# Optimization experiments

Measured on AMD Instinct MI355X. Metric: run time of the kernel, lower is better.

Reference implementation:

```python
import jax, jax.numpy as jnp
import numpy as np

D_MODEL = 1024
D_STATE = 16
D_CONV = 4
EXPAND = 2
D_INNER = EXPAND * D_MODEL  # 2048
BATCH = 2
SEQ = 2048


def setup_inputs() -> dict:
    key = jax.random.key(0)
    ks = jax.random.split(key, 7)
    s = 0.02
    x = jax.random.normal(ks[0], (BATCH, SEQ, D_MODEL), jnp.float32)
    in_proj_w = jax.random.normal(ks[1], (2 * D_INNER, D_MODEL), jnp.float32) * s
    conv_w = jax.random.normal(ks[2], (D_INNER, 1, D_CONV), jnp.float32) * s  # depthwise: groups=d_inner
    conv_b = jnp.zeros((D_INNER,), jnp.float32)
    x_proj_w = jax.random.normal(ks[3], (2 * D_STATE, D_INNER), jnp.float32) * s
    dt_proj_w = jax.random.normal(ks[4], (D_INNER, D_INNER), jnp.float32) * s
    dt_proj_b = jnp.zeros((D_INNER,), jnp.float32)
    # A = arange(1..d_state) repeated for each inner channel; A_log = log(A)
    A_log = jnp.log(jnp.tile(jnp.arange(1, D_STATE + 1, dtype=jnp.float32), (D_INNER, 1)))
    D_param = jnp.ones((D_INNER,), jnp.float32)
    out_proj_w = jax.random.normal(ks[5], (D_MODEL, D_INNER), jnp.float32) * s
    return {"x": x, "in_proj_w": in_proj_w, "conv_w": conv_w, "conv_b": conv_b,
            "x_proj_w": x_proj_w, "dt_proj_w": dt_proj_w, "dt_proj_b": dt_proj_b,
            "A_log": A_log, "D_param": D_param, "out_proj_w": out_proj_w}


def reference(x, in_proj_w, conv_w, conv_b, x_proj_w, dt_proj_w, dt_proj_b, A_log, D_param, out_proj_w):
    B, L, _ = x.shape
    # input projection -> [B, L, 2*d_inner], split into ssm path and gate
    xz = x @ in_proj_w.T
    x_ssm, z = jnp.split(xz, 2, axis=-1)

    # causal depthwise conv1d (torch pads both sides by d_conv-1 then slices [:L])
    xc = jnp.transpose(x_ssm, (0, 2, 1))  # [B, d_inner, L]
    xc = jnp.pad(xc, ((0, 0), (0, 0), (D_CONV - 1, 0)))
    xc = jax.lax.conv_general_dilated(
        xc, conv_w, window_strides=(1,), padding='VALID',
        dimension_numbers=('NCH', 'OIH', 'NCH'), feature_group_count=D_INNER)
    xc = xc + conv_b[None, :, None]
    x_act = jax.nn.silu(jnp.transpose(xc, (0, 2, 1)))  # [B, L, d_inner]

    delta = jax.nn.softplus(x_act @ dt_proj_w.T + dt_proj_b)  # [B, L, d_inner]
    bc = x_act @ x_proj_w.T                                   # [B, L, 2*d_state]
    B_p, C_p = jnp.split(bc, 2, axis=-1)

    A = -jnp.exp(A_log)  # [d_inner, d_state]

    def step(h, inp):
        u_i, d_i, B_i, C_i = inp  # [B,d], [B,d], [B,n], [B,n]
        dA = jnp.exp(d_i[..., None] * A)                       # [B, d, n]
        h = dA * h + (d_i * u_i)[..., None] * B_i[:, None, :]  # [B, d, n]
        y = jnp.einsum('bdn,bn->bd', h, C_i)
        return h, y

    h0 = jnp.zeros((B, D_INNER, D_STATE), x.dtype)
    seq = (jnp.swapaxes(x_act, 0, 1), jnp.swapaxes(delta, 0, 1),
           jnp.swapaxes(B_p, 0, 1), jnp.swapaxes(C_p, 0, 1))
    _, ys = jax.lax.scan(step, h0, seq)  # ys: [L, B, d_inner]
    y_ssm = jnp.swapaxes(ys, 0, 1) + x_act * D_param

    y = y_ssm * jax.nn.silu(z)
    return y @ out_proj_w.T
```

## Files before the change

### kernel.cpp

```cpp
#include <hip/hip_runtime.h>
#include <hip/hip_bf16.h>
#include <math.h>

#define DM 1024
#define DS 16
#define DI 2048
#define NB 2
#define LL 2048
#define BL (NB*LL)
#define LC 32
#define NC (LL/LC)

typedef __attribute__((ext_vector_type(8))) short short8;
typedef __attribute__((ext_vector_type(8))) unsigned short ushort8;
typedef __attribute__((ext_vector_type(4))) float f32x4;

__device__ __forceinline__ float silu_f(float x){ return x / (1.f + __expf(-x)); }
__device__ __forceinline__ float softplus_f(float x){ return (x > 15.f) ? x : log1pf(__expf(x)); }
__device__ __forceinline__ unsigned short f2bf(float f){
  unsigned u = __float_as_uint(f);
  u += 0x7fff + ((u >> 16) & 1);
  return (unsigned short)(u >> 16);
}
__device__ __forceinline__ float bf2f(unsigned short v){
  return __uint_as_float(((unsigned)v) << 16);
}

__global__ __launch_bounds__(256) void f2b_k(const float* __restrict__ src,
                                             unsigned short* __restrict__ dst, int n)
{
  int i = (blockIdx.x * 256 + threadIdx.x) * 8;
  if (i >= n) return;
  float4 v0 = *(const float4*)&src[i];
  float4 v1 = *(const float4*)&src[i + 4];
  ushort8 o;
  o[0]=f2bf(v0.x); o[1]=f2bf(v0.y); o[2]=f2bf(v0.z); o[3]=f2bf(v0.w);
  o[4]=f2bf(v1.x); o[5]=f2bf(v1.y); o[6]=f2bf(v1.z); o[7]=f2bf(v1.w);
  *(ushort8*)&dst[i] = o;
}

__global__ __launch_bounds__(256) void f2b_multi(
    const float* __restrict__ s0, unsigned short* __restrict__ d0, int c0,
    const float* __restrict__ s1, unsigned short* __restrict__ d1, int c1,
    const float* __restrict__ s2, unsigned short* __restrict__ d2, int c2,
    const float* __restrict__ s3, unsigned short* __restrict__ d3, int c3)
{
  int b = blockIdx.x;
  const float* s; unsigned short* d;
  if (b < c0)              { s = s0; d = d0; }
  else if ((b -= c0) < c1) { s = s1; d = d1; }
  else if ((b -= c1) < c2) { s = s2; d = d2; }
  else                     { b -= c2; s = s3; d = d3; }
  int i = (b * 256 + threadIdx.x) * 8;
  float4 v0 = *(const float4*)&s[i];
  float4 v1 = *(const float4*)&s[i + 4];
  ushort8 o;
  o[0]=f2bf(v0.x); o[1]=f2bf(v0.y); o[2]=f2bf(v0.z); o[3]=f2bf(v0.w);
  o[4]=f2bf(v1.x); o[5]=f2bf(v1.y); o[6]=f2bf(v1.z); o[7]=f2bf(v1.w);
  *(ushort8*)&d[i] = o;
}

template<int EPI, int OUTBF>
__global__ __launch_bounds__(512, 1) void gemm5(
    const unsigned short* __restrict__ A, const unsigned short* __restrict__ Bw,
    const float* __restrict__ bias, void* __restrict__ Cp,
    int N, int K)
{
  constexpr int BM = 128, BN = 256;
  __shared__ unsigned short lds[2][(BM + BN) * 64];
  const int t0 = threadIdx.x;
  const int wid = t0 >> 6, lane = t0 & 63;
  const int nbx = N / BN;
  const int cpx = (int)gridDim.x >> 3;
  const int bid = (int)blockIdx.x;
  const int swz = (bid & 7) * cpx + (bid >> 3);
  const int bm = (swz / nbx) * BM, bn = (swz % nbx) * BN;
  const int wm = (wid >> 2) * 64, wn = (wid & 3) * 64;

  f32x4 acc[4][4] = {};

  auto stage = [&](int buf, int kt) {
    const int k0 = kt * 64;
    #pragma unroll
    for (int s = 0; s < 6; s++) {
      int g = wid * 6 + s;
      int row = g * 8 + (lane >> 3);
      int ch  = (lane & 7) ^ (lane >> 3);
      const unsigned short* src;
      if (g < 16) src = A  + (size_t)(bm + row) * K + k0 + ch * 8;
      else        src = Bw + (size_t)(bn + row - BM) * K + k0 + ch * 8;
      __builtin_amdgcn_global_load_lds(
          (const __attribute__((address_space(1))) void*)src,
          (__attribute__((address_space(3))) void*)(&lds[buf][(size_t)g * 512]), 16, 0, 0);
    }
  };

  stage(0, 0);
  stage(1, 1);
  asm volatile("s_waitcnt vmcnt(6)" ::: "memory");
  __builtin_amdgcn_s_barrier();

  const int nk = K >> 6;

#define G5_READS(Q)                                                          \
  short8 af[2][4], bfr[2][4];                                                \
  _Pragma("unroll")                                                          \
  for (int ks = 0; ks < 2; ks++) {                                           \
    int cc = ((ks << 2) + (lane >> 4)) ^ (lane & 7);                         \
    _Pragma("unroll")                                                        \
    for (int i = 0; i < 4; i++) {                                            \
      af[ks][i]  = *(const short8*)&lds[Q][(wm + i * 16 + (lane & 15)) * 64 + cc * 8]; \
      bfr[ks][i] = *(const short8*)&lds[Q][BM * 64 + (wn + i * 16 + (lane & 15)) * 64 + cc * 8]; \
    }                                                                        \
  }

#define G5_MFMA()                                                            \
  _Pragma("unroll")                                                          \
  for (int ks = 0; ks < 2; ks++)                                             \
    _Pragma("unroll")                                                        \
    for (int i = 0; i < 4; i++)                                              \
      _Pragma("unroll")                                                      \
      for (int j = 0; j < 4; j++)                                            \
        acc[i][j] = __builtin_amdgcn_mfma_f32_16x16x32_bf16(af[ks][i], bfr[ks][j], acc[i][j], 0, 0, 0);

  for (int t = 0; t < nk - 2; t++) {
    const int q = t & 1;
    G5_READS(q)
    asm volatile("s_waitcnt lgkmcnt(0)" ::: "memory");
    __builtin_amdgcn_sched_barrier(0);
    __builtin_amdgcn_s_barrier();
    stage(q, t + 2);
    __builtin_amdgcn_sched_barrier(0);
    G5_MFMA()
    __builtin_amdgcn_sched_barrier(0);
    asm volatile("s_waitcnt vmcnt(6)" ::: "memory");
    __builtin_amdgcn_s_barrier();
  }
  {
    const int q = (nk - 2) & 1;
    G5_READS(q)
    G5_MFMA()
    __builtin_amdgcn_sched_barrier(0);
    asm volatile("s_waitcnt vmcnt(0)" ::: "memory");
    __builtin_amdgcn_s_barrier();
  }
  {
    const int q = (nk - 1) & 1;
    G5_READS(q)
    G5_MFMA()
  }
#undef G5_READS
#undef G5_MFMA

  #pragma unroll
  for (int i = 0; i < 4; i++) {
    #pragma unroll
    for (int j = 0; j < 4; j++) {
      int col = bn + wn + j * 16 + (lane & 15);
      float bv = (EPI == 1) ? bias[col] : 0.f;
      #pragma unroll
      for (int r = 0; r < 4; r++) {
        int row = bm + wm + i * 16 + (lane >> 4) * 4 + r;
        float v = acc[i][j][r];
        if (EPI == 1) v = softplus_f(v + bv);
        if (OUTBF) ((unsigned short*)Cp)[(size_t)row * N + col] = f2bf(v);
        else       ((float*)Cp)[(size_t)row * N + col] = v;
      }
    }
  }
}

__global__ __launch_bounds__(256) void conv_silu_k(
    const unsigned short* __restrict__ xz, const float* __restrict__ cw,
    const float* __restrict__ cb, unsigned short* __restrict__ xa)
{
  int v = blockIdx.x * 256 + threadIdx.x;
  int d8 = (v & (DI/8 - 1)) * 8;
  int bl = v >> 8;
  int l  = bl & (LL - 1);
  float acc[8];
  #pragma unroll
  for (int j = 0; j < 8; j++) acc[j] = cb[d8 + j];
  size_t rowb = (size_t)bl * (2 * DI) + d8;
  #pragma unroll
  for (int k = 0; k < 4; k++) {
    int ls = l - 3 + k;
    if (ls >= 0) {
      ushort8 xv = *(const ushort8*)&xz[rowb + (size_t)(k - 3) * (2 * DI)];
      #pragma unroll
      for (int j = 0; j < 8; j++) acc[j] += bf2f(xv[j]) * cw[(d8 + j) * 4 + k];
    }
  }
  ushort8 o;
  #pragma unroll
  for (int j = 0; j < 8; j++) o[j] = f2bf(silu_f(acc[j]));
  *(ushort8*)&xa[(size_t)bl * DI + d8] = o;
}

__global__ __launch_bounds__(256) void bc_k(
    const unsigned short* __restrict__ xa, const unsigned short* __restrict__ w,
    float* __restrict__ bc)
{
  __shared__ unsigned short sx[8 * DI];
  const int t = threadIdx.x;
  const size_t base = (size_t)blockIdx.x * 8 * DI;
  #pragma unroll
  for (int it = 0; it < 8; it++) {
    int v = t + it * 256;
    *(ushort8*)&sx[v * 8] = *(const ushort8*)&xa[base + (size_t)v * 8];
  }
  __syncthreads();
  const int m = t >> 5, n = t & 31;
  const unsigned short* wr = w + (size_t)n * DI;
  const unsigned short* xr = sx + m * DI;
  float acc = 0.f;
  #pragma unroll 4
  for (int k = 0; k < DI; k += 8) {
    ushort8 xv = *(const ushort8*)&xr[k];
    ushort8 wv = *(const ushort8*)&wr[k];
    #pragma unroll
    for (int j = 0; j < 8; j++) acc += bf2f(xv[j]) * bf2f(wv[j]);
  }
  bc[(size_t)(blockIdx.x * 8 + m) * 32 + n] = acc;
}

__global__ __launch_bounds__(256) void scan_part1(
    const float* __restrict__ dlt, const unsigned short* __restrict__ xa,
    const float* __restrict__ bc, const float* __restrict__ A_log,
    float* __restrict__ S_arr, float* __restrict__ sumdlt)
{
  const int bid = blockIdx.x;
  const int b = bid >> 9;
  const int c = (bid >> 3) & (NC - 1);
  const int dg = bid & 7;
  const int t = threadIdx.x;
  const int d = dg * 256 + t;
  float Ac[16];
  #pragma unroll
  for (int n = 0; n < 16; n++) Ac[n] = -__expf(A_log[d * 16 + n]);
  __shared__ float sB[LC][16];
  for (int e = t; e < LC * 16; e += 256) {
    int l = e >> 4, n = e & 15;
    sB[l][n] = bc[(size_t)(b * LL + c * LC + l) * 32 + n];
  }
  __syncthreads();
  float h[16] = {};
  float sd = 0.f;
  size_t rowbase = (size_t)(b * LL + c * LC) * DI + d;
  for (int l = 0; l < LC; l++) {
    float dl = dlt[rowbase + (size_t)l * DI];
    float u  = bf2f(xa[rowbase + (size_t)l * DI]);
    float w = dl * u;
    sd += dl;
    #pragma unroll
    for (int n = 0; n < 16; n++) {
      float dA = __expf(dl * Ac[n]);
      h[n] = dA * h[n] + w * sB[l][n];
    }
  }
  float* Sp = S_arr + ((size_t)(b * NC + c) * DI + d) * 16;
  #pragma unroll
  for (int n = 0; n < 16; n++) Sp[n] = h[n];
  sumdlt[(size_t)(b * NC + c) * DI + d] = sd;
}

__global__ __launch_bounds__(256) void scan_combine(
    const float* __restrict__ A_log, const float* __restrict__ sumdlt,
    float* __restrict__ S_arr)
{
  int tid = blockIdx.x * 256 + threadIdx.x;
  int n = tid & 15;
  int d = (tid >> 4) & (DI - 1);
  int b = tid >> 15;
  float Ac = -__expf(A_log[d * 16 + n]);
  float h = 0.f;
  for (int c = 0; c < NC; c++) {
    size_t idx = ((size_t)(b * NC + c) * DI + d) * 16 + n;
    float S = S_arr[idx];
    float P = __expf(sumdlt[(size_t)(b * NC + c) * DI + d] * Ac);
    S_arr[idx] = h;
    h = P * h + S;
  }
}

__global__ __launch_bounds__(256) void scan_part2(
    const float* __restrict__ dlt, const unsigned short* __restrict__ xa,
    const float* __restrict__ bc, const float* __restrict__ A_log,
    const float* __restrict__ Dp, const unsigned short* __restrict__ xz,
    const float* __restrict__ Hin, unsigned short* __restrict__ y)
{
  const int bid = blockIdx.x;
  const int b = bid >> 9;
  const int c = (bid >> 3) & (NC - 1);
  const int dg = bid & 7;
  const int t = threadIdx.x;
  const int d = dg * 256 + t;
  float Ac[16];
  #pragma unroll
  for (int n = 0; n < 16; n++) Ac[n] = -__expf(A_log[d * 16 + n]);
  __shared__ float sB[LC][16];
  __shared__ float sC[LC][16];
  for (int e = t; e < LC * 16; e += 256) {
    int l = e >> 4, n = e & 15;
    size_t row = (size_t)(b * LL + c * LC + l) * 32;
    sB[l][n] = bc[row + n];
    sC[l][n] = bc[row + 16 + n];
  }
  __syncthreads();
  float h[16];
  const float* Hp = Hin + ((size_t)(b * NC + c) * DI + d) * 16;
  #pragma unroll
  for (int n = 0; n < 16; n++) h[n] = Hp[n];
  const float Dv = Dp[d];
  size_t rowbase = (size_t)(b * LL + c * LC) * DI + d;
  for (int l = 0; l < LC; l++) {
    float dl = dlt[rowbase + (size_t)l * DI];
    float u  = bf2f(xa[rowbase + (size_t)l * DI]);
    float w = dl * u;
    float ya = 0.f;
    #pragma unroll
    for (int n = 0; n < 16; n++) {
      float dA = __expf(dl * Ac[n]);
      h[n] = dA * h[n] + w * sB[l][n];
      ya += h[n] * sC[l][n];
    }
    float zz = bf2f(xz[(size_t)(b * LL + c * LC + l) * (2 * DI) + DI + d]);
    y[rowbase + (size_t)l * DI] = f2bf((ya + u * Dv) * silu_f(zz));
  }
}

extern "C" void kernel_launch(void* const* d_in, const int* in_sizes, int n_in,
                              void* d_out, int out_size, void* d_ws, size_t ws_size,
                              hipStream_t stream)
{
  const float* x    = (const float*)d_in[0];
  const float* Win  = (const float*)d_in[1];
  const float* cw   = (const float*)d_in[2];
  const float* cb   = (const float*)d_in[3];
  const float* Wxp  = (const float*)d_in[4];
  const float* Wdt  = (const float*)d_in[5];
  const float* bdt  = (const float*)d_in[6];
  const float* Alog = (const float*)d_in[7];
  const float* Dp   = (const float*)d_in[8];
  const float* Wout = (const float*)d_in[9];
  float* out = (float*)d_out;

  float* ws = (float*)d_ws;
  float* dlt    = ws;
  float* bcb    = dlt + 8388608;
  float* S_arr  = bcb + 131072;
  float* sumdlt = S_arr + 4194304;
  unsigned short* xz_bf = (unsigned short*)(sumdlt + 262144);
  unsigned short* xa_bf = xz_bf + 16777216;
  unsigned short* y_bf  = xa_bf + 8388608;
  unsigned short* x_bf  = y_bf;
  unsigned short* win_bf= y_bf + 4194304;
  unsigned short* wbuf  = y_bf + 8388608;
  unsigned short* wxp_bf= wbuf + 4194304;

  f2b_multi<<<dim3(2048 + 2048 + 2048 + 32), dim3(256), 0, stream>>>(
      x, x_bf, 2048, Win, win_bf, 2048, Wdt, wbuf, 2048, Wxp, wxp_bf, 32);
  gemm5<0,1><<<dim3(512), dim3(512), 0, stream>>>(x_bf, win_bf, nullptr, xz_bf, 2*DI, DM);
  conv_silu_k<<<dim3(BL*DI/8/256), dim3(256), 0, stream>>>(xz_bf, cw, cb, xa_bf);
  gemm5<1,0><<<dim3(256), dim3(512), 0, stream>>>(xa_bf, wbuf, bdt, dlt, DI, DI);
  f2b_k<<<dim3(DM*DI/2048), dim3(256), 0, stream>>>(Wout, wbuf, DM*DI);
  bc_k<<<dim3(BL/8), dim3(256), 0, stream>>>(xa_bf, wxp_bf, bcb);
  scan_part1<<<dim3(NB*NC*8), dim3(256), 0, stream>>>(dlt, xa_bf, bcb, Alog, S_arr, sumdlt);
  scan_combine<<<dim3(NB*DI*DS/256), dim3(256), 0, stream>>>(Alog, sumdlt, S_arr);
  scan_part2<<<dim3(NB*NC*8), dim3(256), 0, stream>>>(dlt, xa_bf, bcb, Alog, Dp, xz_bf, S_arr, y_bf);
  gemm5<0,0><<<dim3(128), dim3(512), 0, stream>>>(y_bf, wbuf, nullptr, out, DM, DI);
}
```

Before: 363.2 us.

## Interleave LDS fragment reads with MFMA clusters and shrink out-proj tile

Restructures the bf16 GEMM main loop so LDS fragment reads for the next k-substep and next tile are issued between quarter-sized MFMA clusters, with s_setprio raising priority around the MFMAs. This software-pipelines LDS latency against matrix math instead of reading everything and then computing. The BN tile width is now a template parameter, and the output projection uses BN=128 with 256 blocks instead of 128 blocks to fill more CUs. Risks include extra barriers, higher register pressure, and a hard-coded unroll-by-two that assumes an even tile count.

```diff
diff --git a/kernel.cpp b/kernel.cpp
--- a/kernel.cpp
+++ b/kernel.cpp
@@ -60,32 +60,39 @@
   *(ushort8*)&d[i] = o;
 }
 
-template<int EPI, int OUTBF>
-__global__ __launch_bounds__(512, 1) void gemm5(
+template<int BN, int EPI, int OUTBF>
+__global__ __launch_bounds__(512, 1) void gemm6(
     const unsigned short* __restrict__ A, const unsigned short* __restrict__ Bw,
     const float* __restrict__ bias, void* __restrict__ Cp,
     int N, int K)
 {
-  constexpr int BM = 128, BN = 256;
+  constexpr int BM = 128;
+  constexpr int WN = BN / 4;
+  constexpr int NRJ = WN / 16;
+  constexpr int NH = NRJ / 2;
+  constexpr int SL = (BM + BN) / 64;
   __shared__ unsigned short lds[2][(BM + BN) * 64];
-  const int t0 = threadIdx.x;
-  const int wid = t0 >> 6, lane = t0 & 63;
+  const int t0i = threadIdx.x;
+  const int wid = t0i >> 6, lane = t0i & 63;
   const int nbx = N / BN;
   const int cpx = (int)gridDim.x >> 3;
   const int bid = (int)blockIdx.x;
   const int swz = (bid & 7) * cpx + (bid >> 3);
   const int bm = (swz / nbx) * BM, bn = (swz % nbx) * BN;
-  const int wm = (wid >> 2) * 64, wn = (wid & 3) * 64;
-
-  f32x4 acc[4][4] = {};
+  const int wm = (wid >> 2) * 64, wn = (wid & 3) * WN;
+  const int ln15 = lane & 15, l16 = lane >> 4, lx7 = lane & 7;
+
+  f32x4 acc[4][NRJ] = {};
+  short8 af[2][4];
+  short8 bfr[2][NH];
 
   auto stage = [&](int buf, int kt) {
     const int k0 = kt * 64;
     #pragma unroll
-    for (int s = 0; s < 6; s++) {
-      int g = wid * 6 + s;
+    for (int s = 0; s < SL; s++) {
+      int g = wid * SL + s;
       int row = g * 8 + (lane >> 3);
-      int ch  = (lane & 7) ^ (lane >> 3);
+      int ch  = lx7 ^ (lane >> 3);
       const unsigned short* src;
       if (g < 16) src = A  + (size_t)(bm + row) * K + k0 + ch * 8;
       else        src = Bw + (size_t)(bn + row - BM) * K + k0 + ch * 8;
@@ -94,73 +101,90 @@
           (__attribute__((address_space(3))) void*)(&lds[buf][(size_t)g * 512]), 16, 0, 0);
     }
   };
-
-  stage(0, 0);
-  stage(1, 1);
-  asm volatile("s_waitcnt vmcnt(6)" ::: "memory");
+  auto read_af = [&](short8* dst, const unsigned short* buf, int ks) {
+    int cc = ((ks << 2) + l16) ^ lx7;
+    #pragma unroll
+    for (int i = 0; i < 4; i++)
+      dst[i] = *(const short8*)&buf[(wm + i * 16 + ln15) * 64 + cc * 8];
+  };
+  auto read_bf = [&](short8* dst, const unsigned short* buf, int ks, int jh) {
+    int cc = ((ks << 2) + l16) ^ lx7;
+    #pragma unroll
+    for (int j = 0; j < NH; j++)
+      dst[j] = *(const short8*)&buf[BM * 64 + (wn + (jh * NH + j) * 16 + ln15) * 64 + cc * 8];
+  };
+  auto cluster = [&](short8* a, short8* b, int jh) {
+    #pragma unroll
+    for (int i = 0; i < 4; i++)
+      #pragma unroll
+      for (int j = 0; j < NH; j++)
+        acc[i][jh * NH + j] = __builtin_amdgcn_mfma_f32_16x16x32_bf16(a[i], b[j], acc[i][jh * NH + j], 0, 0, 0);
+  };
+
+#define SB    __builtin_amdgcn_sched_barrier(0)
+#define LGKM0 asm volatile("s_waitcnt lgkmcnt(0)" ::: "memory")
+#define PRIO1 __builtin_amdgcn_s_setprio(1)
+#define PRIO0 __builtin_amdgcn_s_setprio(0)
+
+#define G6_TILE(T, Q, STG, VMN)                                              \
+  { const unsigned short* bq  = &lds[Q][0];                                  \
+    const unsigned short* bq1 = &lds[(Q) ^ 1][0];                            \
+                                                                     \
+    read_bf(bfr[1], bq, 0, 1); SB;                                           \
+    PRIO1; cluster(af[0], bfr[0], 0); PRIO0; LGKM0; SB;                      \
+                                                                     \
+    read_af(af[1], bq, 1); read_bf(bfr[0], bq, 1, 0); SB;                    \
+    PRIO1; cluster(af[0], bfr[1], 1); PRIO0; LGKM0; SB;                      \
+                                                                     \
+    read_bf(bfr[1], bq, 1, 1); SB;                                           \
+    PRIO1; cluster(af[1], bfr[0], 0); PRIO0; LGKM0; SB;                      \
+                                                                     \
+    __builtin_amdgcn_s_barrier();                                            \
+    if (STG) stage(Q, (T) + 2);                                              \
+    asm volatile("s_waitcnt vmcnt(%0)" :: "n"(VMN) : "memory"); SB;          \
+    __builtin_amdgcn_s_barrier();                                            \
+    read_af(af[0], bq1, 0); read_bf(bfr[0], bq1, 0, 0); SB;                  \
+    PRIO1; cluster(af[1], bfr[1], 1); PRIO0; LGKM0; SB; }
+
+  const int nk = K >> 6;
+
+  stage(0, 0); stage(1, 1);
+  asm volatile("s_waitcnt vmcnt(%0)" :: "n"(SL) : "memory");
   __builtin_amdgcn_s_barrier();
-
-  const int nk = K >> 6;
-
-#define G5_READS(Q)                                                          \
-  short8 af[2][4], bfr[2][4];                                                \
-  _Pragma("unroll")                                                          \
-  for (int ks = 0; ks < 2; ks++) {                                           \
-    int cc = ((ks << 2) + (lane >> 4)) ^ (lane & 7);                         \
-    _Pragma("unroll")                                                        \
-    for (int i = 0; i < 4; i++) {                                            \
-      af[ks][i]  = *(const short8*)&lds[Q][(wm + i * 16 + (lane & 15)) * 64 + cc * 8]; \
-      bfr[ks][i] = *(const short8*)&lds[Q][BM * 64 + (wn + i * 16 + (lane & 15)) * 64 + cc * 8]; \
-    }                                                                        \
-  }
-
-#define G5_MFMA()                                                            \
-  _Pragma("unroll")                                                          \
-  for (int ks = 0; ks < 2; ks++)                                             \
-    _Pragma("unroll")                                                        \
-    for (int i = 0; i < 4; i++)                                              \
-      _Pragma("unroll")                                                      \
-      for (int j = 0; j < 4; j++)                                            \
-        acc[i][j] = __builtin_amdgcn_mfma_f32_16x16x32_bf16(af[ks][i], bfr[ks][j], acc[i][j], 0, 0, 0);
-
-  for (int t = 0; t < nk - 2; t++) {
-    const int q = t & 1;
-    G5_READS(q)
-    asm volatile("s_waitcnt lgkmcnt(0)" ::: "memory");
-    __builtin_amdgcn_sched_barrier(0);
-    __builtin_amdgcn_s_barrier();
-    stage(q, t + 2);
-    __builtin_amdgcn_sched_barrier(0);
-    G5_MFMA()
-    __builtin_amdgcn_sched_barrier(0);
-    asm volatile("s_waitcnt vmcnt(6)" ::: "memory");
-    __builtin_amdgcn_s_barrier();
-  }
+  read_af(af[0], &lds[0][0], 0); read_bf(bfr[0], &lds[0][0], 0, 0);
+  LGKM0; SB;
+
+  for (int tp = 0; tp < (nk - 2) / 2; ++tp) {
+    const int tv = tp * 2;
+    G6_TILE(tv, 0, true, SL)
+    G6_TILE(tv + 1, 1, true, SL)
+  }
+  G6_TILE(nk - 2, 0, false, 0)
   {
-    const int q = (nk - 2) & 1;
-    G5_READS(q)
-    G5_MFMA()
-    __builtin_amdgcn_sched_barrier(0);
-    asm volatile("s_waitcnt vmcnt(0)" ::: "memory");
-    __builtin_amdgcn_s_barrier();
-  }
-  {
-    const int q = (nk - 1) & 1;
-    G5_READS(q)
-    G5_MFMA()
-  }
-#undef G5_READS
-#undef G5_MFMA
+    const unsigned short* b1 = &lds[1][0];
+    read_bf(bfr[1], b1, 0, 1); SB;
+    PRIO1; cluster(af[0], bfr[0], 0); PRIO0; LGKM0; SB;
+    read_af(af[1], b1, 1); read_bf(bfr[0], b1, 1, 0); SB;
+    PRIO1; cluster(af[0], bfr[1], 1); PRIO0; LGKM0; SB;
+    read_bf(bfr[1], b1, 1, 1); SB;
+    PRIO1; cluster(af[1], bfr[0], 0); PRIO0; LGKM0; SB;
+    PRIO1; cluster(af[1], bfr[1], 1); PRIO0;
+  }
+#undef G6_TILE
+#undef SB
+#undef LGKM0
+#undef PRIO1
+#undef PRIO0
 
   #pragma unroll
   for (int i = 0; i < 4; i++) {
     #pragma unroll
-    for (int j = 0; j < 4; j++) {
-      int col = bn + wn + j * 16 + (lane & 15);
+    for (int j = 0; j < NRJ; j++) {
+      int col = bn + wn + j * 16 + ln15;
       float bv = (EPI == 1) ? bias[col] : 0.f;
       #pragma unroll
       for (int r = 0; r < 4; r++) {
-        int row = bm + wm + i * 16 + (lane >> 4) * 4 + r;
+        int row = bm + wm + i * 16 + l16 * 4 + r;
         float v = acc[i][j][r];
         if (EPI == 1) v = softplus_f(v + bv);
         if (OUTBF) ((unsigned short*)Cp)[(size_t)row * N + col] = f2bf(v);
@@ -360,13 +384,13 @@
 
   f2b_multi<<<dim3(2048 + 2048 + 2048 + 32), dim3(256), 0, stream>>>(
       x, x_bf, 2048, Win, win_bf, 2048, Wdt, wbuf, 2048, Wxp, wxp_bf, 32);
-  gemm5<0,1><<<dim3(512), dim3(512), 0, stream>>>(x_bf, win_bf, nullptr, xz_bf, 2*DI, DM);
+  gemm6<256,0,1><<<dim3(512), dim3(512), 0, stream>>>(x_bf, win_bf, nullptr, xz_bf, 2*DI, DM);
   conv_silu_k<<<dim3(BL*DI/8/256), dim3(256), 0, stream>>>(xz_bf, cw, cb, xa_bf);
-  gemm5<1,0><<<dim3(256), dim3(512), 0, stream>>>(xa_bf, wbuf, bdt, dlt, DI, DI);
+  gemm6<256,1,0><<<dim3(256), dim3(512), 0, stream>>>(xa_bf, wbuf, bdt, dlt, DI, DI);
   f2b_k<<<dim3(DM*DI/2048), dim3(256), 0, stream>>>(Wout, wbuf, DM*DI);
   bc_k<<<dim3(BL/8), dim3(256), 0, stream>>>(xa_bf, wxp_bf, bcb);
   scan_part1<<<dim3(NB*NC*8), dim3(256), 0, stream>>>(dlt, xa_bf, bcb, Alog, S_arr, sumdlt);
   scan_combine<<<dim3(NB*DI*DS/256), dim3(256), 0, stream>>>(Alog, sumdlt, S_arr);
   scan_part2<<<dim3(NB*NC*8), dim3(256), 0, stream>>>(dlt, xa_bf, bcb, Alog, Dp, xz_bf, S_arr, y_bf);
-  gemm5<0,0><<<dim3(128), dim3(512), 0, stream>>>(y_bf, wbuf, nullptr, out, DM, DI);
-}
+  gemm6<128,0,0><<<dim3(256), dim3(512), 0, stream>>>(y_bf, wbuf, nullptr, out, DM, DI);
+}
```

Measured after the change: 341.1 us. 1.06x faster.

## Replace double-buffered 128x256 GEMM with single-buffer 128x128 tile kernel

Applied to the files above, without the earlier changes.

Swaps the 512-thread, 128x256-tile, double-buffered GEMM with explicit waitcnt pipelining for a 256-thread, 128x128-tile kernel. The new kernel uses one LDS buffer and two __syncthreads per k-step, so loads are not overlapped with MFMA inside a block. Grids double, and the smaller LDS footprint and no occupancy cap let more blocks share a CU. The intent is to rely on cross-block occupancy rather than intra-block prefetch. The cost is more global traffic per output from the smaller tiles and no software pipelining.

```diff
diff --git a/kernel.cpp b/kernel.cpp
--- a/kernel.cpp
+++ b/kernel.cpp
@@ -61,106 +61,69 @@
 }
 
 template<int EPI, int OUTBF>
-__global__ __launch_bounds__(512, 1) void gemm5(
+__global__ __launch_bounds__(256) void gemm7(
     const unsigned short* __restrict__ A, const unsigned short* __restrict__ Bw,
     const float* __restrict__ bias, void* __restrict__ Cp,
     int N, int K)
 {
-  constexpr int BM = 128, BN = 256;
-  __shared__ unsigned short lds[2][(BM + BN) * 64];
-  const int t0 = threadIdx.x;
-  const int wid = t0 >> 6, lane = t0 & 63;
-  const int nbx = N / BN;
+  __shared__ unsigned short lds[256 * 64];
+  const int t = threadIdx.x;
+  const int wid = t >> 6, lane = t & 63;
+  const int nbx = N >> 7;
   const int cpx = (int)gridDim.x >> 3;
   const int bid = (int)blockIdx.x;
   const int swz = (bid & 7) * cpx + (bid >> 3);
-  const int bm = (swz / nbx) * BM, bn = (swz % nbx) * BN;
-  const int wm = (wid >> 2) * 64, wn = (wid & 3) * 64;
+  const int bm = (swz / nbx) << 7, bn = (swz % nbx) << 7;
+  const int wm = (wid >> 1) * 64, wn = (wid & 1) * 64;
+  const int ln15 = lane & 15, l16 = lane >> 4, lx7 = lane & 7;
+  const int srow = lane >> 3;
+  const int sch  = lx7 ^ srow;
 
   f32x4 acc[4][4] = {};
 
-  auto stage = [&](int buf, int kt) {
-    const int k0 = kt * 64;
-    #pragma unroll
-    for (int s = 0; s < 6; s++) {
-      int g = wid * 6 + s;
-      int row = g * 8 + (lane >> 3);
-      int ch  = (lane & 7) ^ (lane >> 3);
+  for (int kt = 0; kt < (K >> 6); kt++) {
+    const int k0 = kt << 6;
+    __syncthreads();
+    #pragma unroll
+    for (int s = 0; s < 8; s++) {
+      int g = wid * 8 + s;
+      int row = g * 8 + srow;
       const unsigned short* src;
-      if (g < 16) src = A  + (size_t)(bm + row) * K + k0 + ch * 8;
-      else        src = Bw + (size_t)(bn + row - BM) * K + k0 + ch * 8;
+      if (g < 16) src = A  + (size_t)(bm + row) * K + k0 + sch * 8;
+      else        src = Bw + (size_t)(bn + row - 128) * K + k0 + sch * 8;
       __builtin_amdgcn_global_load_lds(
           (const __attribute__((address_space(1))) void*)src,
-          (__attribute__((address_space(3))) void*)(&lds[buf][(size_t)g * 512]), 16, 0, 0);
-    }
-  };
-
-  stage(0, 0);
-  stage(1, 1);
-  asm volatile("s_waitcnt vmcnt(6)" ::: "memory");
-  __builtin_amdgcn_s_barrier();
-
-  const int nk = K >> 6;
-
-#define G5_READS(Q)                                                          \
-  short8 af[2][4], bfr[2][4];                                                \
-  _Pragma("unroll")                                                          \
-  for (int ks = 0; ks < 2; ks++) {                                           \
-    int cc = ((ks << 2) + (lane >> 4)) ^ (lane & 7);                         \
-    _Pragma("unroll")                                                        \
-    for (int i = 0; i < 4; i++) {                                            \
-      af[ks][i]  = *(const short8*)&lds[Q][(wm + i * 16 + (lane & 15)) * 64 + cc * 8]; \
-      bfr[ks][i] = *(const short8*)&lds[Q][BM * 64 + (wn + i * 16 + (lane & 15)) * 64 + cc * 8]; \
-    }                                                                        \
-  }
-
-#define G5_MFMA()                                                            \
-  _Pragma("unroll")                                                          \
-  for (int ks = 0; ks < 2; ks++)                                             \
-    _Pragma("unroll")                                                        \
-    for (int i = 0; i < 4; i++)                                              \
-      _Pragma("unroll")                                                      \
-      for (int j = 0; j < 4; j++)                                            \
-        acc[i][j] = __builtin_amdgcn_mfma_f32_16x16x32_bf16(af[ks][i], bfr[ks][j], acc[i][j], 0, 0, 0);
-
-  for (int t = 0; t < nk - 2; t++) {
-    const int q = t & 1;
-    G5_READS(q)
-    asm volatile("s_waitcnt lgkmcnt(0)" ::: "memory");
-    __builtin_amdgcn_sched_barrier(0);
-    __builtin_amdgcn_s_barrier();
-    stage(q, t + 2);
-    __builtin_amdgcn_sched_barrier(0);
-    G5_MFMA()
-    __builtin_amdgcn_sched_barrier(0);
-    asm volatile("s_waitcnt vmcnt(6)" ::: "memory");
-    __builtin_amdgcn_s_barrier();
-  }
-  {
-    const int q = (nk - 2) & 1;
-    G5_READS(q)
-    G5_MFMA()
-    __builtin_amdgcn_sched_barrier(0);
-    asm volatile("s_waitcnt vmcnt(0)" ::: "memory");
-    __builtin_amdgcn_s_barrier();
-  }
-  {
-    const int q = (nk - 1) & 1;
-    G5_READS(q)
-    G5_MFMA()
-  }
-#undef G5_READS
-#undef G5_MFMA
+          (__attribute__((address_space(3))) void*)(&lds[g * 512]), 16, 0, 0);
+    }
+    __syncthreads();
+    short8 af[2][4], bfr[2][4];
+    #pragma unroll
+    for (int ks = 0; ks < 2; ks++) {
+      int cc = ((ks << 2) + l16) ^ lx7;
+      #pragma unroll
+      for (int i = 0; i < 4; i++) {
+        af[ks][i]  = *(const short8*)&lds[(wm + i * 16 + ln15) * 64 + cc * 8];
+        bfr[ks][i] = *(const short8*)&lds[(128 + wn + i * 16 + ln15) * 64 + cc * 8];
+      }
+    }
+    #pragma unroll
+    for (int ks = 0; ks < 2; ks++)
+      #pragma unroll
+      for (int i = 0; i < 4; i++)
+        #pragma unroll
+        for (int j = 0; j < 4; j++)
+          acc[i][j] = __builtin_amdgcn_mfma_f32_16x16x32_bf16(af[ks][i], bfr[ks][j], acc[i][j], 0, 0, 0);
+  }
 
   #pragma unroll
   for (int i = 0; i < 4; i++) {
     #pragma unroll
     for (int j = 0; j < 4; j++) {
-      int col = bn + wn + j * 16 + (lane & 15);
+      int col = bn + wn + j * 16 + ln15;
       float bv = (EPI == 1) ? bias[col] : 0.f;
       #pragma unroll
       for (int r = 0; r < 4; r++) {
-        int row = bm + wm + i * 16 + (lane >> 4) * 4 + r;
+        int row = bm + wm + i * 16 + l16 * 4 + r;
         float v = acc[i][j][r];
         if (EPI == 1) v = softplus_f(v + bv);
         if (OUTBF) ((unsigned short*)Cp)[(size_t)row * N + col] = f2bf(v);
@@ -360,13 +323,13 @@
 
   f2b_multi<<<dim3(2048 + 2048 + 2048 + 32), dim3(256), 0, stream>>>(
       x, x_bf, 2048, Win, win_bf, 2048, Wdt, wbuf, 2048, Wxp, wxp_bf, 32);
-  gemm5<0,1><<<dim3(512), dim3(512), 0, stream>>>(x_bf, win_bf, nullptr, xz_bf, 2*DI, DM);
+  gemm7<0,1><<<dim3(1024), dim3(256), 0, stream>>>(x_bf, win_bf, nullptr, xz_bf, 2*DI, DM);
   conv_silu_k<<<dim3(BL*DI/8/256), dim3(256), 0, stream>>>(xz_bf, cw, cb, xa_bf);
-  gemm5<1,0><<<dim3(256), dim3(512), 0, stream>>>(xa_bf, wbuf, bdt, dlt, DI, DI);
+  gemm7<1,0><<<dim3(512), dim3(256), 0, stream>>>(xa_bf, wbuf, bdt, dlt, DI, DI);
   f2b_k<<<dim3(DM*DI/2048), dim3(256), 0, stream>>>(Wout, wbuf, DM*DI);
   bc_k<<<dim3(BL/8), dim3(256), 0, stream>>>(xa_bf, wxp_bf, bcb);
   scan_part1<<<dim3(NB*NC*8), dim3(256), 0, stream>>>(dlt, xa_bf, bcb, Alog, S_arr, sumdlt);
   scan_combine<<<dim3(NB*DI*DS/256), dim3(256), 0, stream>>>(Alog, sumdlt, S_arr);
   scan_part2<<<dim3(NB*NC*8), dim3(256), 0, stream>>>(dlt, xa_bf, bcb, Alog, Dp, xz_bf, S_arr, y_bf);
-  gemm5<0,0><<<dim3(128), dim3(512), 0, stream>>>(y_bf, wbuf, nullptr, out, DM, DI);
-}
+  gemm7<0,0><<<dim3(256), dim3(256), 0, stream>>>(y_bf, wbuf, nullptr, out, DM, DI);
+}
```

New measurement: 382.0 us. 1.05x slower.
